# Kernel tuning notes

Measured on AMD Instinct MI355X. Metric: run time of the kernel, lower is better.

## Reference

```python
import jax, jax.numpy as jnp
import numpy as np

D_MODEL = 1024
N_HEADS = 16
D_K = D_MODEL // N_HEADS
D_FF = 4096
EPS = 1e-6


def _layernorm(x, g, b):
    mu = jnp.mean(x, axis=-1, keepdims=True)
    var = jnp.mean(jnp.square(x - mu), axis=-1, keepdims=True)
    return (x - mu) * jax.lax.rsqrt(var + EPS) * g + b


def setup_inputs() -> dict:
    key = jax.random.key(0)
    ks = jax.random.split(key, 12)
    B, S = 2, 2048
    sd_attn = (1.0 / np.sqrt(2.0)) * np.sqrt(2.0 / (D_MODEL + D_MODEL))  # xavier gain 1/sqrt(2) (std approx)
    sd_ff1 = np.sqrt(2.0 / (D_MODEL + D_FF))
    sd_ff2 = np.sqrt(2.0 / (D_FF + D_MODEL))
    return {
        "x": jax.random.normal(ks[0], (B, S, D_MODEL), jnp.float32),
        "mask": jnp.ones((B, S), jnp.int32),
        # weights stored (in, out) so forward is x @ W
        "wq": jax.random.normal(ks[1], (D_MODEL, D_MODEL), jnp.float32) * sd_attn,
        "wk": jax.random.normal(ks[2], (D_MODEL, D_MODEL), jnp.float32) * sd_attn,
        "wv": jax.random.normal(ks[3], (D_MODEL, D_MODEL), jnp.float32) * sd_attn,
        "wo": jax.random.normal(ks[4], (D_MODEL, D_MODEL), jnp.float32) * sd_attn,
        "wo_b": jnp.zeros((D_MODEL,), jnp.float32),
        "w1": jax.random.normal(ks[5], (D_MODEL, D_FF), jnp.float32) * sd_ff1,
        "b1": jnp.zeros((D_FF,), jnp.float32),
        "w2": jax.random.normal(ks[6], (D_FF, D_MODEL), jnp.float32) * sd_ff2,
        "b2": jnp.zeros((D_MODEL,), jnp.float32),
        "g1": jnp.ones((D_MODEL,), jnp.float32),
        "be1": jnp.zeros((D_MODEL,), jnp.float32),
        "g2": jnp.ones((D_MODEL,), jnp.float32),
        "be2": jnp.zeros((D_MODEL,), jnp.float32),
    }


def reference(x, mask, wq, wk, wv, wo, wo_b, w1, b1, w2, b2, g1, be1, g2, be2):
    B, S, _ = x.shape
    scale = 1.0 / np.sqrt(D_K)
    # project and split heads -> [B, H, S, Dk]
    q = (x @ wq).reshape(B, S, N_HEADS, D_K).transpose(0, 2, 1, 3)
    k = (x @ wk).reshape(B, S, N_HEADS, D_K).transpose(0, 2, 1, 3)
    v = (x @ wv).reshape(B, S, N_HEADS, D_K).transpose(0, 2, 1, 3)
    scores = jnp.einsum("bhqd,bhkd->bhqk", q, k) * scale  # [B,H,S,S]
    m = (mask[:, None, None, :] == 0)
    scores = jnp.where(m, -1e9, scores)
    attn = jax.nn.softmax(scores, axis=-1)
    ctx = jnp.einsum("bhqk,bhkd->bhqd", attn, v)
    ctx = ctx.transpose(0, 2, 1, 3).reshape(B, S, D_MODEL)
    attn_out = ctx @ wo + wo_b
    x = _layernorm(x + attn_out, g1, be1)
    ff = jax.nn.gelu(x @ w1 + b1, approximate=False) @ w2 + b2
    return _layernorm(x + ff, g2, be2)
```

## Files before the change

### kernel.cpp

```cpp
#include <hip/hip_runtime.h>
#include <cstdint>

#define DEVINL __device__ __forceinline__

typedef __attribute__((ext_vector_type(8))) short short8;
typedef __attribute__((ext_vector_type(4))) short short4v;
typedef __attribute__((ext_vector_type(4))) float floatx4;
typedef __attribute__((ext_vector_type(4))) unsigned short ushort4v;

DEVINL uint32_t pkbf(float a, float b) {
  uint32_t d;
  asm("v_cvt_pk_bf16_f32 %0, %1, %2" : "=v"(d) : "v"(a), "v"(b));
  return d;
}
DEVINL unsigned short f2bf(float f) {
  union { float f; uint32_t u; } v; v.f = f;
  return (unsigned short)((v.u + 0x7fffu + ((v.u >> 16) & 1u)) >> 16);
}
DEVINL float bf2f(unsigned short h) {
  union { uint32_t u; float f; } v; v.u = ((uint32_t)h) << 16;
  return v.f;
}

#if defined(__has_builtin) && __has_builtin(__builtin_amdgcn_exp2f)
#define EXP2(x) __builtin_amdgcn_exp2f(x)
#else
#define EXP2(x) exp2f(x)
#endif

DEVINL float fast_gelu(float v) {
  const float z = -2.30220795f * v * (1.0f + 0.044715f * v * v);
  return v * __builtin_amdgcn_rcpf(1.0f + EXP2(z));
}

typedef __attribute__((address_space(3))) unsigned char* lds_ptr_t;
typedef const __attribute__((address_space(1))) unsigned char* gbl_ptr_t;
DEVINL void load_lds_128(const void* g, void* l) {
  __builtin_amdgcn_global_load_lds((gbl_ptr_t)g, (lds_ptr_t)l, 16, 0, 0);
}

#define MFMA16(a, b, c) __builtin_amdgcn_mfma_f32_16x16x32_bf16((a), (b), (c), 0, 0, 0)

#define QSCALE2 0.18033688011112042f

__global__ __launch_bounds__(256) void prep_kernel(
    const float* __restrict__ x, unsigned short* __restrict__ XB,
    const float* __restrict__ wq, const float* __restrict__ wk,
    const float* __restrict__ wv, const float* __restrict__ wo,
    unsigned short* __restrict__ WQKV, unsigned short* __restrict__ WOT,
    const float* __restrict__ w1, unsigned short* __restrict__ W1T,
    const float* __restrict__ w2, unsigned short* __restrict__ W2T,
    const int* __restrict__ mask, unsigned short* __restrict__ MB) {
  const int bid = blockIdx.x;
  if (bid >= 16384) {
    const int i0 = threadIdx.x * 16;
#pragma unroll
    for (int j = 0; j < 16; ++j) MB[i0 + j] = mask[i0 + j] ? 0x3F80 : 0;
    return;
  }
  if (bid < 4096) {
    const int i = (bid * 256 + threadIdx.x) * 4;
    floatx4 v = *(const floatx4*)(x + i);
    union { uint32_t u[2]; ushort4v v4; } o;
    o.u[0] = pkbf(v[0], v[1]);
    o.u[1] = pkbf(v[2], v[3]);
    *(ushort4v*)(XB + i) = o.v4;
    return;
  }
  const float* in;
  unsigned short* out;
  int K, N, bx, by;
  if (bid < 8192) {
    const int b2 = bid - 4096, z = b2 >> 10;
    in = (z == 0) ? wq : (z == 1) ? wk : (z == 2) ? wv : wo;
    out = (z == 3) ? WOT : WQKV + (size_t)z * 1024 * 1024;
    K = 1024; N = 1024; bx = b2 & 31; by = (b2 >> 5) & 31;
  } else if (bid < 12288) {
    const int b3 = bid - 8192;
    in = w1; out = W1T; K = 1024; N = 4096; bx = b3 & 127; by = b3 >> 7;
  } else {
    const int b4 = bid - 12288;
    in = w2; out = W2T; K = 4096; N = 1024; bx = b4 & 31; by = b4 >> 5;
  }
  __shared__ float tile[32][33];
  const int n0 = bx * 32, k0 = by * 32;
  const int tx = threadIdx.x & 31, ty = threadIdx.x >> 5;
#pragma unroll
  for (int i = 0; i < 4; ++i)
    tile[ty + 8 * i][tx] = in[(size_t)(k0 + ty + 8 * i) * N + n0 + tx];
  __syncthreads();
#pragma unroll
  for (int i = 0; i < 4; ++i)
    out[(size_t)(n0 + ty + 8 * i) * K + k0 + tx] = f2bf(tile[tx][ty + 8 * i]);
}

template <int EPI, int SK>
__global__ __launch_bounds__(256, 3) void gemm_bt_kernel(
    const unsigned short* __restrict__ A, const unsigned short* __restrict__ BT,
    const float* __restrict__ bias, void* __restrict__ C0, void* __restrict__ C1,
    void* __restrict__ C2, int M, int N, int K, const int* __restrict__ msk) {
  __shared__ __align__(16) unsigned short As[128 * 64];
  __shared__ __align__(16) unsigned short Bs[128 * 64];
  const int tid = threadIdx.x;
  const int w = tid >> 6, l = tid & 63;
  const int lq = l >> 4, lr = l & 15;
  const int m0 = blockIdx.y * 128, n0 = blockIdx.x * 128;
  const int wm = (w >> 1) * 64, wn = (w & 1) * 64;
  const int r_a = l >> 2;
  const int colb = (l & 3) * 8;
  const int kslice = K / SK;
  const int kbeg = kslice * blockIdx.z;
  const int region = (EPI == 5) ? (n0 >> 10) : 0;

  uint32_t mbits = 0xFFFFu;
  if (EPI == 5 && region == 2) {
    mbits = 0;
#pragma unroll
    for (int mt = 0; mt < 4; ++mt) {
      const int4 m4 = *(const int4*)(msk + m0 + wm + mt * 16 + lq * 4);
      mbits |= (m4.x ? 1u : 0u) << (mt * 4);
      mbits |= (m4.y ? 1u : 0u) << (mt * 4 + 1);
      mbits |= (m4.z ? 1u : 0u) << (mt * 4 + 2);
      mbits |= (m4.w ? 1u : 0u) << (mt * 4 + 3);
    }
  }

  floatx4 acc[4][4];
  const floatx4 fz = {0.f, 0.f, 0.f, 0.f};
#pragma unroll
  for (int mt = 0; mt < 4; ++mt)
#pragma unroll
    for (int nt = 0; nt < 4; ++nt) acc[mt][nt] = fz;

  for (int k0 = kbeg; k0 < kbeg + kslice; k0 += 64) {
    __syncthreads();
#pragma unroll
    for (int p = 0; p < 2; ++p) {
#pragma unroll
      for (int i = 0; i < 2; ++i) {
        const int c = w * 2 + i;
        load_lds_128(A + (size_t)(m0 + c * 16 + r_a) * K + k0 + p * 32 + colb,
                     (char*)As + p * 8192 + c * 1024);
        load_lds_128(BT + (size_t)(n0 + c * 16 + r_a) * K + k0 + p * 32 + colb,
                     (char*)Bs + p * 8192 + c * 1024);
      }
    }
    __syncthreads();
#pragma unroll
    for (int p = 0; p < 2; ++p) {
      short8 af[4], bf[4];
#pragma unroll
      for (int mt = 0; mt < 4; ++mt)
        af[mt] = *(const short8*)((const char*)As + p * 8192 + (wm + mt * 16 + lr) * 64 + lq * 16);
#pragma unroll
      for (int nt = 0; nt < 4; ++nt)
        bf[nt] = *(const short8*)((const char*)Bs + p * 8192 + (wn + nt * 16 + lr) * 64 + lq * 16);
#pragma unroll
      for (int mt = 0; mt < 4; ++mt)
#pragma unroll
        for (int nt = 0; nt < 4; ++nt)
          acc[mt][nt] = MFMA16(af[mt], bf[nt], acc[mt][nt]);
    }
  }

  void* Cp = (SK > 1 && blockIdx.z) ? C1 : C0;
#pragma unroll
  for (int mt = 0; mt < 4; ++mt) {
#pragma unroll
    for (int nt = 0; nt < 4; ++nt) {
      const int n = n0 + wn + nt * 16 + lr;
      float bval = 0.f;
      if (EPI == 2) bval = bias[n];
#pragma unroll
      for (int r = 0; r < 4; ++r) {
        const int m = m0 + wm + mt * 16 + lq * 4 + r;
        float v = acc[mt][nt][r];
        if (EPI == 4) {
          ((unsigned short*)Cp)[(size_t)m * N + n] = f2bf(v);
        } else if (EPI == 2) {
          ((unsigned short*)C0)[(size_t)m * N + n] = f2bf(fast_gelu(v + bval));
        } else {
          if (region == 0) {
            ((unsigned short*)C0)[(size_t)m * 1024 + n] = f2bf(v * QSCALE2);
          } else if (region == 1) {
            ((unsigned short*)C1)[(size_t)m * 1024 + (n - 1024)] = f2bf(v);
          } else {
            const int nn = n - 2048;
            const int bidx = m >> 11, s = m & 2047;
            const int u = s & 31;
            const int sp = (s & ~31) | (u & 3) | (((u >> 4) & 1) << 2) | (((u >> 2) & 3) << 3);
            const int hh = nn >> 6, d = nn & 63;
            const float vv = ((mbits >> (mt * 4 + r)) & 1u) ? v : 0.f;
            ((unsigned short*)C2)[((size_t)((bidx * 16 + hh) * 64 + d)) * 2048 + sp] = f2bf(vv);
          }
        }
      }
    }
  }
}

__global__ __launch_bounds__(256, 4) void flash_kernel(
    const unsigned short* __restrict__ Q, const unsigned short* __restrict__ Kg,
    const unsigned short* __restrict__ VT, const unsigned short* __restrict__ MB,
    unsigned short* __restrict__ ctx) {
  __shared__ __align__(16) unsigned short Ks[128 * 64];
  __shared__ __align__(16) unsigned short VTs[64 * 128];

  const int tid = threadIdx.x, w = tid >> 6, l = tid & 63;
  const int lq = l >> 4, lr = l & 15;
  const int lin = blockIdx.x;
  const int xcd = lin & 7, slot = lin >> 3;
  const int bh = xcd * 4 + (slot >> 5);
  const int b = bh >> 4, h = bh & 15;
  const int q0 = (slot & 31) * 64;

  const unsigned short* Qp = Q + (size_t)(b * 2048 + q0) * 1024 + h * 64;
  const unsigned short* Kp = Kg + (size_t)(b * 2048) * 1024 + h * 64;
  const unsigned short* VTp = VT + (size_t)bh * 64 * 2048;
  const unsigned short* mbp = MB + b * 2048;

  {
    const int rq = l >> 3, cs = l & 7;
#pragma unroll
    for (int i = 0; i < 2; ++i) {
      const int c = w * 2 + i;
      load_lds_128(Qp + (size_t)(c * 8 + rq) * 1024 + cs * 8, (char*)Ks + c * 1024);
    }
  }
  __syncthreads();
  short8 qf[2];
  qf[0] = *(const short8*)((const char*)Ks + (w * 16 + lr) * 128 + lq * 16);
  qf[1] = *(const short8*)((const char*)Ks + (w * 16 + lr) * 128 + 64 + lq * 16);

  const floatx4 fz = {0.f, 0.f, 0.f, 0.f};
  floatx4 o[4] = {fz, fz, fz, fz};
  floatx4 l_acc = fz;

  const int krow = l >> 3, kslot = l & 7;
  const int vrow = l >> 4, vslot = l & 15;

  for (int kb = 0; kb < 2048; kb += 128) {
    __syncthreads();
#pragma unroll
    for (int i = 0; i < 4; ++i) {
      const int c4 = w * 4 + i;
      {
        const int row = c4 * 8 + krow;
        const int cc = kslot ^ (row & 7);
        load_lds_128(Kp + (size_t)(kb + row) * 1024 + cc * 8, (char*)Ks + c4 * 1024);
      }
      {
        const int row = c4 * 4 + vrow;
        const int cc = vslot ^ (row & 15);
        load_lds_128(VTp + (size_t)row * 2048 + kb + cc * 8, (char*)VTs + c4 * 1024);
      }
    }
    short8 mf[4];
#pragma unroll
    for (int t = 0; t < 4; ++t) {
      const short4v ma = *(const short4v*)(mbp + kb + t * 32 + lq * 4);
      const short4v mb2 = *(const short4v*)(mbp + kb + t * 32 + 16 + lq * 4);
      mf[t] = short8{ma[0], ma[1], ma[2], ma[3], mb2[0], mb2[1], mb2[2], mb2[3]};
    }
    __syncthreads();

#pragma unroll
    for (int h2 = 0; h2 < 2; ++h2) {
      floatx4 s[4];
#pragma unroll
      for (int gg = 0; gg < 4; ++gg) {
        const int g = h2 * 4 + gg;
        const char* rowp = (const char*)Ks + (g * 16 + lr) * 128;
        short8 k0 = *(const short8*)(rowp + ((lq) ^ (lr & 7)) * 16);
        short8 k1 = *(const short8*)(rowp + ((4 + lq) ^ (lr & 7)) * 16);
        floatx4 t = MFMA16(k0, qf[0], fz);
        s[gg] = MFMA16(k1, qf[1], t);
      }
      short8 pf[2];
#pragma unroll
      for (int tt = 0; tt < 2; ++tt) {
        const floatx4 sL = s[tt * 2], sH = s[tt * 2 + 1];
        union { uint32_t u[4]; short8 s8; } pk;
        pk.u[0] = pkbf(EXP2(sL[0]), EXP2(sL[1]));
        pk.u[1] = pkbf(EXP2(sL[2]), EXP2(sL[3]));
        pk.u[2] = pkbf(EXP2(sH[0]), EXP2(sH[1]));
        pk.u[3] = pkbf(EXP2(sH[2]), EXP2(sH[3]));
        pf[tt] = pk.s8;
      }
#pragma unroll
      for (int tt = 0; tt < 2; ++tt) {
        const int t = h2 * 2 + tt;
        l_acc = MFMA16(pf[tt], mf[t], l_acc);
#pragma unroll
        for (int nt = 0; nt < 4; ++nt) {
          const int d = nt * 16 + lr;
          short8 vf = *(const short8*)((const char*)VTs + d * 256 +
                                       (((t * 4 + lq) ^ (d & 15)) * 16));
          o[nt] = MFMA16(pf[tt], vf, o[nt]);
        }
      }
    }
  }

#pragma unroll
  for (int r = 0; r < 4; ++r) {
    const float inv = 1.0f / l_acc[r];
    const int q = q0 + w * 16 + lq * 4 + r;
#pragma unroll
    for (int nt = 0; nt < 4; ++nt)
      ctx[(size_t)(b * 2048 + q) * 1024 + h * 64 + nt * 16 + lr] = f2bf(o[nt][r] * inv);
  }
}

template <int RESBF, int OUTBF>
__global__ __launch_bounds__(256) void ln2_kernel(
    const void* __restrict__ res, const unsigned short* __restrict__ y0,
    const unsigned short* __restrict__ y1, const float* __restrict__ bias,
    const float* __restrict__ gamma, const float* __restrict__ beta,
    void* __restrict__ outp) {
  const int row = blockIdx.x, t = threadIdx.x;
  const size_t base = (size_t)row * 1024 + t * 4;
  float v[4];
  if (RESBF) {
    ushort4v r4 = *(const ushort4v*)((const unsigned short*)res + base);
#pragma unroll
    for (int j = 0; j < 4; ++j) v[j] = bf2f(r4[j]);
  } else {
    floatx4 r4 = *(const floatx4*)((const float*)res + base);
#pragma unroll
    for (int j = 0; j < 4; ++j) v[j] = r4[j];
  }
  const ushort4v a4 = *(const ushort4v*)(y0 + base);
  const ushort4v b4v = *(const ushort4v*)(y1 + base);
  const floatx4 bi4 = *(const floatx4*)(bias + t * 4);
  float s = 0.f, ss = 0.f;
#pragma unroll
  for (int j = 0; j < 4; ++j) {
    v[j] += bf2f(a4[j]) + bf2f(b4v[j]) + bi4[j];
    s += v[j];
    ss += v[j] * v[j];
  }
#pragma unroll
  for (int off = 1; off < 64; off <<= 1) {
    s += __shfl_xor(s, off);
    ss += __shfl_xor(ss, off);
  }
  __shared__ float red[8];
  const int w = t >> 6;
  if ((t & 63) == 0) { red[w] = s; red[4 + w] = ss; }
  __syncthreads();
  s = red[0] + red[1] + red[2] + red[3];
  ss = red[4] + red[5] + red[6] + red[7];
  const float mean = s * (1.0f / 1024.0f);
  const float var = ss * (1.0f / 1024.0f) - mean * mean;
  const float rstd = rsqrtf(var + 1e-6f);
  const floatx4 g4 = *(const floatx4*)(gamma + t * 4);
  const floatx4 be4 = *(const floatx4*)(beta + t * 4);
  if (OUTBF) {
    union { uint32_t u[2]; ushort4v v4; } o;
    o.u[0] = pkbf((v[0] - mean) * rstd * g4[0] + be4[0],
                  (v[1] - mean) * rstd * g4[1] + be4[1]);
    o.u[1] = pkbf((v[2] - mean) * rstd * g4[2] + be4[2],
                  (v[3] - mean) * rstd * g4[3] + be4[3]);
    *(ushort4v*)((unsigned short*)outp + base) = o.v4;
  } else {
    floatx4 o;
#pragma unroll
    for (int j = 0; j < 4; ++j) o[j] = (v[j] - mean) * rstd * g4[j] + be4[j];
    *(floatx4*)((float*)outp + base) = o;
  }
}

extern "C" void kernel_launch(void* const* d_in, const int* in_sizes, int n_in,
                              void* d_out, int out_size, void* d_ws, size_t ws_size,
                              hipStream_t stream) {
  (void)in_sizes; (void)n_in; (void)out_size; (void)ws_size;
  const float* x    = (const float*)d_in[0];
  const int*   mask = (const int*)d_in[1];
  const float* wq   = (const float*)d_in[2];
  const float* wk   = (const float*)d_in[3];
  const float* wv   = (const float*)d_in[4];
  const float* wo   = (const float*)d_in[5];
  const float* wo_b = (const float*)d_in[6];
  const float* w1   = (const float*)d_in[7];
  const float* b1   = (const float*)d_in[8];
  const float* w2   = (const float*)d_in[9];
  const float* b2   = (const float*)d_in[10];
  const float* g1   = (const float*)d_in[11];
  const float* be1  = (const float*)d_in[12];
  const float* g2   = (const float*)d_in[13];
  const float* be2  = (const float*)d_in[14];
  float* out = (float*)d_out;

  char* ws = (char*)d_ws;
  const size_t MBy = 1024ull * 1024ull;
  unsigned short* WQKV = (unsigned short*)(ws + 0 * MBy);
  unsigned short* WOT  = (unsigned short*)(ws + 6 * MBy);
  unsigned short* W1T  = (unsigned short*)(ws + 8 * MBy);
  unsigned short* W2T  = (unsigned short*)(ws + 16 * MBy);
  unsigned short* XB   = (unsigned short*)(ws + 24 * MBy);
  unsigned short* Qb   = (unsigned short*)(ws + 32 * MBy);
  unsigned short* Kb   = (unsigned short*)(ws + 40 * MBy);
  unsigned short* VTb  = (unsigned short*)(ws + 48 * MBy);
  unsigned short* CTX  = (unsigned short*)(ws + 56 * MBy);
  unsigned short* ATT0 = (unsigned short*)(ws + 32 * MBy);
  unsigned short* ATT1 = (unsigned short*)(ws + 40 * MBy);
  unsigned short* Hb   = (unsigned short*)(ws + 24 * MBy);
  unsigned short* G1   = (unsigned short*)(ws + 32 * MBy);
  unsigned short* FF20 = (unsigned short*)(ws + 64 * MBy);
  unsigned short* FF21 = (unsigned short*)(ws + 72 * MBy);
  unsigned short* MB   = (unsigned short*)(ws + 78 * MBy);

  prep_kernel<<<16385, 256, 0, stream>>>(x, XB, wq, wk, wv, wo, WQKV, WOT,
                                         w1, W1T, w2, W2T, mask, MB);
  gemm_bt_kernel<5, 1><<<dim3(24, 32), 256, 0, stream>>>(
      XB, WQKV, nullptr, Qb, Kb, VTb, 4096, 3072, 1024, mask);
  flash_kernel<<<1024, 256, 0, stream>>>(Qb, Kb, VTb, MB, CTX);
  gemm_bt_kernel<4, 2><<<dim3(8, 32, 2), 256, 0, stream>>>(
      CTX, WOT, nullptr, ATT0, ATT1, nullptr, 4096, 1024, 1024, nullptr);
  ln2_kernel<0, 1><<<4096, 256, 0, stream>>>(x, ATT0, ATT1, wo_b, g1, be1, Hb);
  gemm_bt_kernel<2, 1><<<dim3(32, 32), 256, 0, stream>>>(
      Hb, W1T, b1, G1, nullptr, nullptr, 4096, 4096, 1024, nullptr);
  gemm_bt_kernel<4, 2><<<dim3(8, 32, 2), 256, 0, stream>>>(
      G1, W2T, nullptr, FF20, FF21, nullptr, 4096, 1024, 4096, nullptr);
  ln2_kernel<1, 0><<<4096, 256, 0, stream>>>(Hb, FF20, FF21, b2, g2, be2, out);
}
```

Before: 329.4 us.

## Process 128 query rows per flash block to reuse K/V tiles across two query groups

Each flash-attention block now handles 128 queries (two 16-row groups per wave) instead of 64, so every K/V tile loaded into LDS feeds twice as many MFMAs. The grid is halved to 512 blocks and launch bounds drop to 2 blocks per CU to allow the doubled accumulator registers. The goal is to cut K/V global and LDS traffic per unit of work, at the cost of fewer blocks and lower occupancy. A sync is added after the Q fragments are read and the first loop sync is skipped.

After: 329.2 us. Within noise of the previous version (-0.0%).

```diff
diff --git a/kernel.cpp b/kernel.cpp
--- a/kernel.cpp
+++ b/kernel.cpp
@@ -199,7 +199,7 @@
   }
 }
 
-__global__ __launch_bounds__(256, 4) void flash_kernel(
+__global__ __launch_bounds__(256, 2) void flash_kernel(
     const unsigned short* __restrict__ Q, const unsigned short* __restrict__ Kg,
     const unsigned short* __restrict__ VT, const unsigned short* __restrict__ MB,
     unsigned short* __restrict__ ctx) {
@@ -210,9 +210,9 @@
   const int lq = l >> 4, lr = l & 15;
   const int lin = blockIdx.x;
   const int xcd = lin & 7, slot = lin >> 3;
-  const int bh = xcd * 4 + (slot >> 5);
+  const int bh = xcd * 4 + (slot >> 4);
   const int b = bh >> 4, h = bh & 15;
-  const int q0 = (slot & 31) * 64;
+  const int q0 = (slot & 15) * 128;
 
   const unsigned short* Qp = Q + (size_t)(b * 2048 + q0) * 1024 + h * 64;
   const unsigned short* Kp = Kg + (size_t)(b * 2048) * 1024 + h * 64;
@@ -222,25 +222,33 @@
   {
     const int rq = l >> 3, cs = l & 7;
 #pragma unroll
-    for (int i = 0; i < 2; ++i) {
-      const int c = w * 2 + i;
+    for (int i = 0; i < 4; ++i) {
+      const int c = w * 4 + i;
       load_lds_128(Qp + (size_t)(c * 8 + rq) * 1024 + cs * 8, (char*)Ks + c * 1024);
     }
   }
   __syncthreads();
-  short8 qf[2];
-  qf[0] = *(const short8*)((const char*)Ks + (w * 16 + lr) * 128 + lq * 16);
-  qf[1] = *(const short8*)((const char*)Ks + (w * 16 + lr) * 128 + 64 + lq * 16);
+  short8 qf[2][2];
+#pragma unroll
+  for (int qg = 0; qg < 2; ++qg) {
+    qf[qg][0] = *(const short8*)((const char*)Ks + (w * 32 + qg * 16 + lr) * 128 + lq * 16);
+    qf[qg][1] = *(const short8*)((const char*)Ks + (w * 32 + qg * 16 + lr) * 128 + 64 + lq * 16);
+  }
+  __syncthreads();
 
   const floatx4 fz = {0.f, 0.f, 0.f, 0.f};
-  floatx4 o[4] = {fz, fz, fz, fz};
-  floatx4 l_acc = fz;
+  floatx4 o[2][4];
+#pragma unroll
+  for (int qg = 0; qg < 2; ++qg)
+#pragma unroll
+    for (int nt = 0; nt < 4; ++nt) o[qg][nt] = fz;
+  floatx4 l_acc[2] = {fz, fz};
 
   const int krow = l >> 3, kslot = l & 7;
   const int vrow = l >> 4, vslot = l & 15;
 
   for (int kb = 0; kb < 2048; kb += 128) {
-    __syncthreads();
+    if (kb) __syncthreads();
 #pragma unroll
     for (int i = 0; i < 4; ++i) {
       const int c4 = w * 4 + i;
@@ -266,50 +274,59 @@
 
 #pragma unroll
     for (int h2 = 0; h2 < 2; ++h2) {
-      floatx4 s[4];
+      floatx4 s[2][4];
 #pragma unroll
       for (int gg = 0; gg < 4; ++gg) {
         const int g = h2 * 4 + gg;
         const char* rowp = (const char*)Ks + (g * 16 + lr) * 128;
         short8 k0 = *(const short8*)(rowp + ((lq) ^ (lr & 7)) * 16);
         short8 k1 = *(const short8*)(rowp + ((4 + lq) ^ (lr & 7)) * 16);
-        floatx4 t = MFMA16(k0, qf[0], fz);
-        s[gg] = MFMA16(k1, qf[1], t);
-      }
-      short8 pf[2];
-#pragma unroll
-      for (int tt = 0; tt < 2; ++tt) {
-        const floatx4 sL = s[tt * 2], sH = s[tt * 2 + 1];
-        union { uint32_t u[4]; short8 s8; } pk;
-        pk.u[0] = pkbf(EXP2(sL[0]), EXP2(sL[1]));
-        pk.u[1] = pkbf(EXP2(sL[2]), EXP2(sL[3]));
-        pk.u[2] = pkbf(EXP2(sH[0]), EXP2(sH[1]));
-        pk.u[3] = pkbf(EXP2(sH[2]), EXP2(sH[3]));
-        pf[tt] = pk.s8;
-      }
+#pragma unroll
+        for (int qg = 0; qg < 2; ++qg) {
+          floatx4 t = MFMA16(k0, qf[qg][0], fz);
+          s[qg][gg] = MFMA16(k1, qf[qg][1], t);
+        }
+      }
+      short8 pf[2][2];
+#pragma unroll
+      for (int qg = 0; qg < 2; ++qg)
+#pragma unroll
+        for (int tt = 0; tt < 2; ++tt) {
+          const floatx4 sL = s[qg][tt * 2], sH = s[qg][tt * 2 + 1];
+          union { uint32_t u[4]; short8 s8; } pk;
+          pk.u[0] = pkbf(EXP2(sL[0]), EXP2(sL[1]));
+          pk.u[1] = pkbf(EXP2(sL[2]), EXP2(sL[3]));
+          pk.u[2] = pkbf(EXP2(sH[0]), EXP2(sH[1]));
+          pk.u[3] = pkbf(EXP2(sH[2]), EXP2(sH[3]));
+          pf[qg][tt] = pk.s8;
+        }
 #pragma unroll
       for (int tt = 0; tt < 2; ++tt) {
         const int t = h2 * 2 + tt;
-        l_acc = MFMA16(pf[tt], mf[t], l_acc);
+        l_acc[0] = MFMA16(pf[0][tt], mf[t], l_acc[0]);
+        l_acc[1] = MFMA16(pf[1][tt], mf[t], l_acc[1]);
 #pragma unroll
         for (int nt = 0; nt < 4; ++nt) {
           const int d = nt * 16 + lr;
           short8 vf = *(const short8*)((const char*)VTs + d * 256 +
                                        (((t * 4 + lq) ^ (d & 15)) * 16));
-          o[nt] = MFMA16(pf[tt], vf, o[nt]);
+          o[0][nt] = MFMA16(pf[0][tt], vf, o[0][nt]);
+          o[1][nt] = MFMA16(pf[1][tt], vf, o[1][nt]);
         }
       }
     }
   }
 
 #pragma unroll
-  for (int r = 0; r < 4; ++r) {
-    const float inv = 1.0f / l_acc[r];
-    const int q = q0 + w * 16 + lq * 4 + r;
-#pragma unroll
-    for (int nt = 0; nt < 4; ++nt)
-      ctx[(size_t)(b * 2048 + q) * 1024 + h * 64 + nt * 16 + lr] = f2bf(o[nt][r] * inv);
-  }
+  for (int qg = 0; qg < 2; ++qg)
+#pragma unroll
+    for (int r = 0; r < 4; ++r) {
+      const float inv = 1.0f / l_acc[qg][r];
+      const int q = q0 + w * 32 + qg * 16 + lq * 4 + r;
+#pragma unroll
+      for (int nt = 0; nt < 4; ++nt)
+        ctx[(size_t)(b * 2048 + q) * 1024 + h * 64 + nt * 16 + lr] = f2bf(o[qg][nt][r] * inv);
+    }
 }
 
 template <int RESBF, int OUTBF>
@@ -415,7 +432,7 @@
                                          w1, W1T, w2, W2T, mask, MB);
   gemm_bt_kernel<5, 1><<<dim3(24, 32), 256, 0, stream>>>(
       XB, WQKV, nullptr, Qb, Kb, VTb, 4096, 3072, 1024, mask);
-  flash_kernel<<<1024, 256, 0, stream>>>(Qb, Kb, VTb, MB, CTX);
+  flash_kernel<<<512, 256, 0, stream>>>(Qb, Kb, VTb, MB, CTX);
   gemm_bt_kernel<4, 2><<<dim3(8, 32, 2), 256, 0, stream>>>(
       CTX, WOT, nullptr, ATT0, ATT1, nullptr, 4096, 1024, 1024, nullptr);
   ln2_kernel<0, 1><<<4096, 256, 0, stream>>>(x, ATT0, ATT1, wo_b, g1, be1, Hb);
```
